# Kernel tuning notes

Measured on AMD Instinct MI355X. Metric: run time of the kernel, lower is better.

Reference implementation:

```python
import jax, jax.numpy as jnp
import numpy as np

B, N, A = 8, 8192, 10   # batch, points, attributes (xyz + normal + 4 extra)
G, M = 512, 32          # num_group, group_size
EPS = 1e-5


def setup_inputs() -> dict:
    key = jax.random.key(0)
    ks = jax.random.split(key, 16)
    w = lambda k, s: jax.random.normal(k, s, jnp.float32) * 0.02
    inp = {"xyz": jax.random.normal(ks[0], (B, N, A), jnp.float32)}
    # Light_T_Net params (conv1 6->64, conv2 64->512, fc 512->36)
    inp["tn_w1"], inp["tn_b1"] = w(ks[1], (64, 6)), jnp.zeros(64, jnp.float32)
    inp["tn_g1"], inp["tn_be1"] = jnp.ones(64, jnp.float32), jnp.zeros(64, jnp.float32)
    inp["tn_w2"], inp["tn_b2"] = w(ks[2], (512, 64)), jnp.zeros(512, jnp.float32)
    inp["tn_g2"], inp["tn_be2"] = jnp.ones(512, jnp.float32), jnp.zeros(512, jnp.float32)
    inp["tn_fw"], inp["tn_fb"] = w(ks[3], (36, 512)), jnp.zeros(36, jnp.float32)
    # Light_PointNet_Encoder convs: A->128->256->512->1024
    for i, (co, ci) in enumerate([(128, A), (256, 128), (512, 256), (1024, 512)], 1):
        inp[f"w{i}"], inp[f"b{i}"] = w(ks[3 + i], (co, ci)), jnp.zeros(co, jnp.float32)
        inp[f"g{i}"], inp[f"be{i}"] = jnp.ones(co, jnp.float32), jnp.zeros(co, jnp.float32)
    return inp


def _bn(x, g, b):
    # training-mode BatchNorm1d: stats over (batch, length) for [BG, n, C]
    m = x.mean((0, 1))
    v = x.var((0, 1))
    return (x - m) * jax.lax.rsqrt(v + EPS) * g + b


def _fps(xyz, npoint):
    # sequential farthest-point sampling (deterministic start index 0)
    coords = xyz[:, :, :3]
    b, n, _ = xyz.shape

    def step(carry, _):
        dist, far = carry
        cen = jnp.take_along_axis(xyz, far[:, None, None], axis=1)  # [B,1,A]
        d = jnp.sum((coords - cen[:, :, :3]) ** 2, -1)              # [B,N]
        dist = jnp.minimum(dist, d)
        return (dist, jnp.argmax(dist, -1)), (far, cen[:, 0, :])

    dist0 = jnp.full((b, n), 1e10, xyz.dtype)
    far0 = jnp.zeros((b,), jnp.int32)
    _, (idx, attrs) = jax.lax.scan(step, (dist0, far0), None, length=npoint)
    return idx.T, attrs.transpose(1, 0, 2)  # [B,G], [B,G,A]


def _forward(xyz, tn_w1, tn_b1, tn_g1, tn_be1, tn_w2, tn_b2, tn_g2, tn_be2,
             tn_fw, tn_fb, w1, b1, g1, be1, w2, b2, g2, be2,
             w3, b3, g3, be3, w4, b4, g4, be4):
    b = xyz.shape[0]
    # ---- Group_for_all_attribute ----
    _, cen = _fps(xyz, G)                                           # [B,G,A]
    # cdist over full attribute dim; squared distance gives identical topk order
    d2 = (jnp.sum(cen ** 2, -1)[:, :, None] + jnp.sum(xyz ** 2, -1)[:, None, :]
          - 2.0 * jnp.einsum('bga,bna->bgn', cen, xyz))             # [B,G,N]
    idx = jax.lax.top_k(-d2, M)[1]                                  # [B,G,M] smallest dists
    nb = xyz[jnp.arange(b)[:, None, None], idx]                     # [B,G,M,A]
    nb = jnp.concatenate([nb[..., :3] - cen[:, :, None, :3], nb[..., 3:]], -1)
    # ---- Light_PointNet_Encoder ----
    pg = nb.reshape(b * G, M, A)
    x6 = pg[:, :, :6]
    # Light_T_Net
    h = jax.nn.relu(_bn(x6 @ tn_w1.T + tn_b1, tn_g1, tn_be1))
    h = jax.nn.relu(_bn(h @ tn_w2.T + tn_b2, tn_g2, tn_be2))
    t = (h.max(1) @ tn_fw.T + tn_fb + jnp.eye(6, dtype=xyz.dtype).reshape(36)).reshape(-1, 6, 6)
    pg = jnp.concatenate([jnp.einsum('bnc,bcd->bnd', x6, t), pg[:, :, 6:]], -1)
    # 1x1 conv stack (= per-point linear) with training-mode BN
    h = jax.nn.relu(_bn(pg @ w1.T + b1, g1, be1))
    h = jax.nn.relu(_bn(h @ w2.T + b2, g2, be2))
    h = jax.nn.relu(_bn(h @ w3.T + b3, g3, be3))
    h = _bn(h @ w4.T + b4, g4, be4)
    return h.max(1).reshape(b, G, -1)                               # [B,G,1024]


def reference(xyz, tn_w1, tn_b1, tn_g1, tn_be1, tn_w2, tn_b2, tn_g2, tn_be2,
              tn_fw, tn_fb, w1, b1, g1, be1, w2, b2, g2, be2,
              w3, b3, g3, be3, w4, b4, g4, be4):
    return _forward(xyz, tn_w1, tn_b1, tn_g1, tn_be1, tn_w2, tn_b2, tn_g2, tn_be2,
                    tn_fw, tn_fb, w1, b1, g1, be1, w2, b2, g2, be2,
                    w3, b3, g3, be3, w4, b4, g4, be4)
```

## Files before the change

kernel.cpp:

```cpp
#include <hip/hip_runtime.h>
#include <hip/hip_bf16.h>

static constexpr int B_  = 8;
static constexpr int N_  = 8192;
static constexpr int A_  = 10;
static constexpr int G_  = 512;
static constexpr int M_  = 32;
static constexpr int S_TOT = B_ * G_ * M_;
static constexpr float EPS_ = 1e-5f;
static constexpr float FMAXV = 3.402823466e+38f;

__device__ __forceinline__ float b2f(__hip_bfloat16 h) { return __bfloat162float(h); }
__device__ __forceinline__ unsigned short f2bs(float f) {
    __hip_bfloat16 h = __float2bfloat16(f);
    return *reinterpret_cast<unsigned short*>(&h);
}

typedef __bf16 bf16x8 __attribute__((ext_vector_type(8)));
typedef float  f32x4  __attribute__((ext_vector_type(4)));

__device__ __forceinline__ unsigned long long shfl_down_u64(unsigned long long v, int off) {
    unsigned lo = (unsigned)v, hi = (unsigned)(v >> 32);
    lo = __shfl_down(lo, off);
    hi = __shfl_down(hi, off);
    return ((unsigned long long)hi << 32) | lo;
}

static constexpr size_t CO_XYZ  = 0;
static constexpr size_t CO_TNW1 = 655360, CO_TNB1 = 655744, CO_TNG1 = 655808, CO_TNBE1 = 655872;
static constexpr size_t CO_TNW2 = 655936, CO_TNB2 = 688704, CO_TNG2 = 689216, CO_TNBE2 = 689728;
static constexpr size_t CO_TNFW = 690240, CO_TNFB = 708672;
static constexpr size_t CO_W1 = 708708, CO_B1 = 709988, CO_G1 = 710116, CO_BE1 = 710244;
static constexpr size_t CO_W2 = 710372, CO_B2 = 743140, CO_G2 = 743396, CO_BE2 = 743652;
static constexpr size_t CO_W3 = 743908, CO_B3 = 874980, CO_G3 = 875492, CO_BE3 = 876004;
static constexpr size_t CO_W4 = 876516, CO_B4 = 1400804, CO_G4 = 1401828, CO_BE4 = 1402852;
static constexpr size_t CO_TOT = 1403876;

static constexpr size_t WB_TNW2 = 0;
static constexpr size_t WB_W2   = 32768;
static constexpr size_t WB_W3   = 65536;
static constexpr size_t WB_W4   = 196608;
static constexpr size_t WB_TOT  = 720896;

#define MB_ (1024ull * 1024ull)
static constexpr size_t OFF_CANON = 0;
static constexpr size_t OFF_CEN   = 6 * MB_;
static constexpr size_t OFF_XSQ   = 6 * MB_ + 256 * 1024;
static constexpr size_t OFF_STATS = 6 * MB_ + 512 * 1024;
static constexpr size_t OFF_COEFF = 6 * MB_ + 576 * 1024;
static constexpr size_t OFF_DUMMY = 6 * MB_ + 640 * 1024;
static constexpr size_t OFF_TMAT  = 6 * MB_ + 768 * 1024;
static constexpr size_t OFF_WBF16 = 8 * MB_;
static constexpr size_t OFF_PG    = 10 * MB_;
static constexpr size_t OFF_TZ1   = 16 * MB_;
static constexpr size_t OFF_TPMAX = 32 * MB_;
static constexpr size_t OFF_TPMIN = 40 * MB_;
static constexpr size_t OFF_Z1    = 16 * MB_;
static constexpr size_t OFF_MM4X  = 16 * MB_;
static constexpr size_t OFF_MM4N  = 32 * MB_;
static constexpr size_t OFF_Z2    = 48 * MB_;
static constexpr size_t OFF_Z3    = 112 * MB_;
static constexpr size_t NEED_A = 240 * MB_;
static constexpr int NCHUNK_ = 8;
static constexpr int CSAMP_  = S_TOT / NCHUNK_;

static constexpr int STF_T1 = 0;
static constexpr int STF_T2 = 128;
static constexpr int STF_M1 = 1152;
static constexpr int STF_M2 = 1408;
static constexpr int STF_M3 = 1920;
static constexpr int STF_M4 = 2944;

struct Ptrs { const void* p[27]; };

__global__ __launch_bounds__(256)
void zero_kernel(float* __restrict__ p, int n)
{
    for (int i = threadIdx.x; i < n; i += 256) p[i] = 0.f;
}

__global__ __launch_bounds__(256)
void convert_kernel(Ptrs ptrs, float* __restrict__ canon)
{
    const size_t gid = (size_t)blockIdx.x * 256 + threadIdx.x;
    if (gid >= CO_TOT) return;
    constexpr size_t offs[28] = {0, 655360, 655744, 655808, 655872, 655936,
        688704, 689216, 689728, 690240, 708672, 708708, 709988, 710116, 710244,
        710372, 743140, 743396, 743652, 743908, 874980, 875492, 876004, 876516,
        1400804, 1401828, 1402852, 1403876};
    int j = 0;
    while (j < 26 && gid >= offs[j + 1]) ++j;
    const size_t loc = gid - offs[j];
    const bool fp32m = (((const unsigned short*)ptrs.p[3])[0] == 0);
    float v;
    if (fp32m) v = ((const float*)ptrs.p[j])[loc];
    else       v = b2f(((const __hip_bfloat16*)ptrs.p[j])[loc]);
    canon[gid] = v;
}

__global__ __launch_bounds__(256)
void wconv_kernel(const float* __restrict__ canon, __hip_bfloat16* __restrict__ wb)
{
    const size_t gid = (size_t)blockIdx.x * 256 + threadIdx.x;
    if (gid >= WB_TOT) return;
    constexpr size_t offs[5] = {0, 32768, 65536, 196608, 720896};
    constexpr size_t co[4]   = {CO_TNW2, CO_W2, CO_W3, CO_W4};
    int j = 0;
    while (j < 3 && gid >= offs[j + 1]) ++j;
    wb[gid] = __float2bfloat16(canon[co[j] + (gid - offs[j])]);
}

__global__ __launch_bounds__(512)
void fps_kernel(const float* __restrict__ xyz, float* __restrict__ cen)
{
    __shared__ unsigned long long red[2][8];
    __shared__ int fidx[G_];

    const int t = threadIdx.x;
    const int b = blockIdx.x;
    const float* xb = xyz + (size_t)b * N_ * A_;

    float px[16], py[16], pz[16], dist[16];
#pragma unroll
    for (int j = 0; j < 16; ++j) {
        const int i = j * 512 + t;
        px[j] = xb[(size_t)i * A_ + 0];
        py[j] = xb[(size_t)i * A_ + 1];
        pz[j] = xb[(size_t)i * A_ + 2];
        dist[j] = 1e10f;
    }
    __syncthreads();

    int far = 0;
    for (int it = 0; it < G_; ++it) {
        if (t == 0) fidx[it] = far;
        const float2 cxy = *reinterpret_cast<const float2*>(xb + (size_t)far * A_);
        const float  cz  = xb[(size_t)far * A_ + 2];

        unsigned long long best = 0;
#pragma unroll
        for (int j = 0; j < 16; ++j) {
            const float dx = px[j] - cxy.x, dy = py[j] - cxy.y, dz = pz[j] - cz;
            const float d = dx * dx + dy * dy + dz * dz;
            const float nd = fminf(dist[j], d);
            dist[j] = nd;
            const unsigned long long pk =
                ((unsigned long long)__float_as_uint(nd) << 32) |
                (unsigned)~(unsigned)(j * 512 + t);
            best = (pk > best) ? pk : best;
        }
#pragma unroll
        for (int off = 32; off; off >>= 1) {
            const unsigned long long o = shfl_down_u64(best, off);
            best = (o > best) ? o : best;
        }
        if ((t & 63) == 0) red[it & 1][t >> 6] = best;
        __syncthreads();
        unsigned long long m = red[it & 1][0];
#pragma unroll
        for (int w = 1; w < 8; ++w) {
            const unsigned long long o = red[it & 1][w];
            m = (o > m) ? o : m;
        }
        far = (int)(~(unsigned)m);
    }
    __syncthreads();
    for (int e = t; e < G_ * A_; e += 512) {
        const int it = e / A_;
        const int a  = e - it * A_;
        cen[((size_t)b * G_ + it) * A_ + a] = xb[(size_t)fidx[it] * A_ + a];
    }
}

__global__ __launch_bounds__(256)
void xsq_kernel(const float* __restrict__ xyz, float* __restrict__ xsq)
{
    const int i = blockIdx.x * 256 + threadIdx.x;
    float s = 0.f;
#pragma unroll
    for (int a = 0; a < A_; ++a) { const float v = xyz[(size_t)i * A_ + a]; s += v * v; }
    xsq[i] = s;
}

__global__ __launch_bounds__(256)
void knn_kernel(const float* __restrict__ xyz, const float* __restrict__ cen,
                const float* __restrict__ xsq, float* __restrict__ pg)
{
    __shared__ float d2[N_];
    __shared__ float ca[A_];
    __shared__ float csqs;
    __shared__ float redV[4];
    __shared__ int   redI[4];
    __shared__ int   win[M_];
    __shared__ int   curwin;

    const int t  = threadIdx.x;
    const int bg = blockIdx.x;
    const int b  = bg >> 9;
    const float* xb  = xyz + (size_t)b * N_ * A_;
    const float* xsb = xsq + (size_t)b * N_;

    if (t < A_) ca[t] = cen[(size_t)bg * A_ + t];
    __syncthreads();
    if (t == 0) {
        float s = 0.f;
        for (int a = 0; a < A_; ++a) s += ca[a] * ca[a];
        csqs = s;
    }
    __syncthreads();
    const float csq = csqs;

    for (int j = 0; j < 32; ++j) {
        const int i = j * 256 + t;
        float dot = 0.f;
#pragma unroll
        for (int a = 0; a < A_; ++a) dot += xb[(size_t)i * A_ + a] * ca[a];
        d2[i] = (csq + xsb[i]) - 2.f * dot;
    }
    __syncthreads();

    float bv = FMAXV; int bi = 0;
    for (int j = 0; j < 32; ++j) {
        const int i = j * 256 + t;
        const float v = d2[i];
        if (v < bv) { bv = v; bi = i; }
    }

    for (int it = 0; it < M_; ++it) {
        float rv = bv; int ri = bi;
#pragma unroll
        for (int off = 32; off; off >>= 1) {
            const float ov = __shfl_down(rv, off);
            const int   oi = __shfl_down(ri, off);
            if (ov < rv || (ov == rv && oi < ri)) { rv = ov; ri = oi; }
        }
        if ((t & 63) == 0) { redV[t >> 6] = rv; redI[t >> 6] = ri; }
        __syncthreads();
        if (t == 0) {
            float v = redV[0]; int wi = redI[0];
            for (int w = 1; w < 4; ++w)
                if (redV[w] < v || (redV[w] == v && redI[w] < wi)) { v = redV[w]; wi = redI[w]; }
            win[it] = wi; curwin = wi; d2[wi] = FMAXV;
        }
        __syncthreads();
        const int wi = curwin;
        if ((wi & 255) == t) {
            bv = FMAXV; bi = 0;
            for (int j = 0; j < 32; ++j) {
                const int i = j * 256 + t;
                const float v = d2[i];
                if (v < bv) { bv = v; bi = i; }
            }
        }
    }
    __syncthreads();
    if (t < M_) {
        const int i = win[t];
        for (int a = 0; a < A_; ++a) {
            float v = xb[(size_t)i * A_ + a];
            if (a < 3) v -= ca[a];
            pg[((size_t)bg * M_ + t) * A_ + a] = v;
        }
    }
}

template<int K, int C>
__global__ __launch_bounds__(256)
void mlp_small_kernel(const float* __restrict__ pgx,
                      const float* __restrict__ W,
                      const float* __restrict__ Bv,
                      __hip_bfloat16* __restrict__ Zout,
                      float* __restrict__ stats)
{
    __shared__ float w[C * K];
    __shared__ float bb[C];
    __shared__ float lstat[C][2];
    const int t = threadIdx.x;
    for (int i = t; i < C * K; i += 256) w[i] = W[i];
    for (int i = t; i < C; i += 256) bb[i] = Bv[i];
    for (int i = t; i < 2 * C; i += 256) ((float*)lstat)[i] = 0.f;
    __syncthreads();

    const size_t s = (size_t)blockIdx.x * 256 + t;
    float x[K];
#pragma unroll
    for (int k = 0; k < K; ++k) x[k] = pgx[s * A_ + k];

    ushort4 u;
    for (int c = 0; c < C; ++c) {
        float z = bb[c];
#pragma unroll
        for (int k = 0; k < K; ++k) z += w[c * K + k] * x[k];
        const unsigned short zs = f2bs(z);
        const int cm = c & 3;
        if (cm == 0) u.x = zs; else if (cm == 1) u.y = zs; else if (cm == 2) u.z = zs;
        else { u.w = zs; *reinterpret_cast<ushort4*>(Zout + s * C + (c - 3)) = u; }

        float sv = z, sq = z * z;
#pragma unroll
        for (int off = 32; off; off >>= 1) {
            sv += __shfl_down(sv, off);
            sq += __shfl_down(sq, off);
        }
        if ((t & 63) == 0) { atomicAdd(&lstat[c][0], sv); atomicAdd(&lstat[c][1], sq); }
    }
    __syncthreads();
    for (int c = t; c < C; c += 256) {
        atomicAdd(&stats[c],     lstat[c][0]);
        atomicAdd(&stats[C + c], lstat[c][1]);
    }
}

__global__ __launch_bounds__(256)
void finalize_kernel(const float* __restrict__ stats, const float* __restrict__ g,
                     const float* __restrict__ be, float* __restrict__ coeff, int C)
{
    for (int c = threadIdx.x; c < C; c += 256) {
        const float mean = stats[c] * (1.f / (float)S_TOT);
        const float var  = stats[C + c] * (1.f / (float)S_TOT) - mean * mean;
        const float sc = g[c] * rsqrtf(fmaxf(var, 0.f) + EPS_);
        coeff[c]     = sc;
        coeff[C + c] = be[c] - mean * sc;
    }
}

template<int K, int N, bool POOL>
__global__ __launch_bounds__(256)
void gemm_mfma_kernel(const __hip_bfloat16* __restrict__ Zin,
                      const float* __restrict__ coeff,
                      const __hip_bfloat16* __restrict__ Wb,
                      const float* __restrict__ Bv,
                      __hip_bfloat16* __restrict__ Zout,
                      float* __restrict__ maxbuf,
                      float* __restrict__ minbuf,
                      float* __restrict__ stats)
{
    constexpr int PITCH = 72;
    __shared__ __hip_bfloat16 As[128 * PITCH];
    __shared__ __hip_bfloat16 Bs[128 * PITCH];
    __shared__ float csc[K];
    __shared__ float csh[K];
    __shared__ float lstat[256];

    const int t    = threadIdx.x;
    const int lane = t & 63;
    const int wave = t >> 6;
    const int wm   = wave >> 1;
    const int wn   = wave & 1;
    const int ln   = lane & 15;
    const int quad = lane >> 4;
    const int c0   = blockIdx.x * 128;
    const int s0   = blockIdx.y * 128;

    for (int i = t; i < K; i += 256) { csc[i] = coeff[i]; csh[i] = coeff[K + i]; }
    lstat[t] = 0.f;

    f32x4 acc[4][4];
#pragma unroll
    for (int ni = 0; ni < 4; ++ni) {
        const float bj = Bv[c0 + wn * 64 + ni * 16 + ln];
#pragma unroll
        for (int mi = 0; mi < 4; ++mi) acc[mi][ni] = (f32x4){bj, bj, bj, bj};
    }

    for (int kt = 0; kt < K; kt += 64) {
        __syncthreads();
#pragma unroll
        for (int p = 0; p < 4; ++p) {
            const int id = p * 256 + t;
            const int r  = id >> 3;
            const int sg = id & 7;
            const float4 raw = *reinterpret_cast<const float4*>(
                Zin + (size_t)(s0 + r) * K + kt + sg * 8);
            const __hip_bfloat162* p2 = reinterpret_cast<const __hip_bfloat162*>(&raw);
            unsigned short tmp[8] __attribute__((aligned(16)));
#pragma unroll
            for (int j = 0; j < 4; ++j) {
                const int k0 = kt + sg * 8 + 2 * j;
                const float x0 = fmaxf(b2f(p2[j].x) * csc[k0]     + csh[k0],     0.f);
                const float x1 = fmaxf(b2f(p2[j].y) * csc[k0 + 1] + csh[k0 + 1], 0.f);
                tmp[2 * j]     = f2bs(x0);
                tmp[2 * j + 1] = f2bs(x1);
            }
            *reinterpret_cast<float4*>(&As[r * PITCH + sg * 8]) =
                *reinterpret_cast<const float4*>(tmp);
            *reinterpret_cast<float4*>(&Bs[r * PITCH + sg * 8]) =
                *reinterpret_cast<const float4*>(Wb + (size_t)(c0 + r) * K + kt + sg * 8);
        }
        __syncthreads();

        bf16x8 af[4][2], bf_[4][2];
#pragma unroll
        for (int mi = 0; mi < 4; ++mi)
#pragma unroll
            for (int kk = 0; kk < 2; ++kk)
                af[mi][kk] = *reinterpret_cast<const bf16x8*>(
                    &As[(wm * 64 + mi * 16 + ln) * PITCH + quad * 8 + kk * 32]);
#pragma unroll
        for (int ni = 0; ni < 4; ++ni)
#pragma unroll
            for (int kk = 0; kk < 2; ++kk)
                bf_[ni][kk] = *reinterpret_cast<const bf16x8*>(
                    &Bs[(wn * 64 + ni * 16 + ln) * PITCH + quad * 8 + kk * 32]);
#pragma unroll
        for (int kk = 0; kk < 2; ++kk)
#pragma unroll
            for (int mi = 0; mi < 4; ++mi)
#pragma unroll
                for (int ni = 0; ni < 4; ++ni)
                    acc[mi][ni] = __builtin_amdgcn_mfma_f32_16x16x32_bf16(
                        af[mi][kk], bf_[ni][kk], acc[mi][ni], 0, 0, 0);
    }

#pragma unroll
    for (int ni = 0; ni < 4; ++ni) {
        float sv = 0.f, sq = 0.f;
#pragma unroll
        for (int mi = 0; mi < 4; ++mi)
#pragma unroll
            for (int r = 0; r < 4; ++r) {
                const float v = acc[mi][ni][r];
                sv += v; sq += v * v;
            }
        sv += __shfl_xor(sv, 16); sq += __shfl_xor(sq, 16);
        sv += __shfl_xor(sv, 32); sq += __shfl_xor(sq, 32);
        if (quad == 0) {
            const int col = wn * 64 + ni * 16 + ln;
            atomicAdd(&lstat[col], sv);
            atomicAdd(&lstat[128 + col], sq);
        }
    }
    __syncthreads();
    if (t < 128) {
        atomicAdd(&stats[c0 + t],     lstat[t]);
        atomicAdd(&stats[N + c0 + t], lstat[128 + t]);
    }

    if constexpr (POOL) {
#pragma unroll
        for (int ni = 0; ni < 4; ++ni) {
            float mx0 = -FMAXV, mn0 = FMAXV, mx1 = -FMAXV, mn1 = FMAXV;
#pragma unroll
            for (int mi = 0; mi < 2; ++mi)
#pragma unroll
                for (int r = 0; r < 4; ++r) {
                    const float v = acc[mi][ni][r];
                    mx0 = fmaxf(mx0, v); mn0 = fminf(mn0, v);
                }
#pragma unroll
            for (int mi = 2; mi < 4; ++mi)
#pragma unroll
                for (int r = 0; r < 4; ++r) {
                    const float v = acc[mi][ni][r];
                    mx1 = fmaxf(mx1, v); mn1 = fminf(mn1, v);
                }
            mx0 = fmaxf(mx0, __shfl_xor(mx0, 16)); mn0 = fminf(mn0, __shfl_xor(mn0, 16));
            mx0 = fmaxf(mx0, __shfl_xor(mx0, 32)); mn0 = fminf(mn0, __shfl_xor(mn0, 32));
            mx1 = fmaxf(mx1, __shfl_xor(mx1, 16)); mn1 = fminf(mn1, __shfl_xor(mn1, 16));
            mx1 = fmaxf(mx1, __shfl_xor(mx1, 32)); mn1 = fminf(mn1, __shfl_xor(mn1, 32));
            if (quad == 0) {
                const int col = c0 + wn * 64 + ni * 16 + ln;
                const int g   = (s0 >> 5) + wm * 2;
                maxbuf[(size_t)g * N + col]       = mx0;
                minbuf[(size_t)g * N + col]       = mn0;
                maxbuf[(size_t)(g + 1) * N + col] = mx1;
                minbuf[(size_t)(g + 1) * N + col] = mn1;
            }
        }
    } else {
#pragma unroll
        for (int mi = 0; mi < 4; ++mi)
#pragma unroll
            for (int r = 0; r < 4; ++r) {
                const size_t row = (size_t)(s0 + wm * 64 + mi * 16 + quad * 4 + r);
#pragma unroll
                for (int ni = 0; ni < 4; ++ni) {
                    const int col = c0 + wn * 64 + ni * 16 + ln;
                    Zout[row * N + col] = __float2bfloat16(acc[mi][ni][r]);
                }
            }
    }
}

__global__ __launch_bounds__(64)
void tnet_fc_kernel(const float* __restrict__ maxbuf, const float* __restrict__ minbuf,
                    const float* __restrict__ coeff, const float* __restrict__ FW,
                    const float* __restrict__ FB, float* __restrict__ tmat)
{
    __shared__ float h[512];
    const int bg = blockIdx.x;
    const int t  = threadIdx.x;
    for (int i = t; i < 512; i += 64) {
        const float sc = coeff[i], sh = coeff[512 + i];
        const float v = (sc >= 0.f) ? maxbuf[(size_t)bg * 512 + i] : minbuf[(size_t)bg * 512 + i];
        h[i] = fmaxf(sc * v + sh, 0.f);
    }
    __syncthreads();
    if (t < 36) {
        float acc = FB[t] + ((t % 7 == 0) ? 1.f : 0.f);
        for (int k = 0; k < 512; ++k) acc += FW[t * 512 + k] * h[k];
        tmat[(size_t)bg * 36 + t] = acc;
    }
}

__global__ __launch_bounds__(256)
void transform_kernel(float* __restrict__ pg, const float* __restrict__ tmat)
{
    const size_t s = (size_t)blockIdx.x * 256 + threadIdx.x;
    const int bg = (int)(s >> 5);
    float x[6];
#pragma unroll
    for (int c = 0; c < 6; ++c) x[c] = pg[s * A_ + c];
    const float* tm = tmat + (size_t)bg * 36;
#pragma unroll
    for (int d = 0; d < 6; ++d) {
        float o = 0.f;
#pragma unroll
        for (int c = 0; c < 6; ++c) o += x[c] * tm[c * 6 + d];
        pg[s * A_ + d] = o;
    }
}

__global__ __launch_bounds__(256)
void output_kernel(const float* __restrict__ maxbuf, const float* __restrict__ minbuf,
                   const float* __restrict__ coeff, const unsigned short* __restrict__ probe,
                   void* __restrict__ out)
{
    const size_t e = (size_t)blockIdx.x * 256 + threadIdx.x;
    const int c = (int)(e & 1023);
    const float sc = coeff[c], sh = coeff[1024 + c];
    const float v = (sc >= 0.f) ? maxbuf[e] : minbuf[e];
    const float r = sc * v + sh;
    if (probe[0] == 0) ((float*)out)[e] = r;
    else ((__hip_bfloat16*)out)[e] = __float2bfloat16(r);
}

extern "C" void kernel_launch(void* const* d_in, const int* in_sizes, int n_in,
                              void* d_out, int out_size, void* d_ws, size_t ws_size,
                              hipStream_t stream)
{
    char* ws = (char*)d_ws;
    float*          canon = (float*)(ws + OFF_CANON);
    float*          cen   = (float*)(ws + OFF_CEN);
    float*          xsq   = (float*)(ws + OFF_XSQ);
    float*          stats = (float*)(ws + OFF_STATS);
    float*          coeff = (float*)(ws + OFF_COEFF);
    float*          dummy = (float*)(ws + OFF_DUMMY);
    float*          tmat  = (float*)(ws + OFF_TMAT);
    __hip_bfloat16* wbf   = (__hip_bfloat16*)(ws + OFF_WBF16);
    float*          tpmax = (float*)(ws + OFF_TPMAX);
    float*          tpmin = (float*)(ws + OFF_TPMIN);
    float*          pg    = (float*)(ws + OFF_PG);
    __hip_bfloat16* tz1   = (__hip_bfloat16*)(ws + OFF_TZ1);
    __hip_bfloat16* z1    = (__hip_bfloat16*)(ws + OFF_Z1);
    __hip_bfloat16* z2    = (__hip_bfloat16*)(ws + OFF_Z2);
    __hip_bfloat16* z3    = (__hip_bfloat16*)(ws + OFF_Z3);
    float*          mmax4 = (float*)(ws + OFF_MM4X);
    float*          mmin4 = (float*)(ws + OFF_MM4N);

    Ptrs ptrs;
    for (int i = 0; i < 27; ++i) ptrs.p[i] = d_in[i];

    const float* cxyz = canon + CO_XYZ;

    zero_kernel<<<1, 256, 0, stream>>>(stats, 5120);
    convert_kernel<<<(int)((CO_TOT + 255) / 256), 256, 0, stream>>>(ptrs, canon);
    wconv_kernel<<<(int)((WB_TOT + 255) / 256), 256, 0, stream>>>(canon, wbf);

    fps_kernel<<<B_, 512, 0, stream>>>(cxyz, cen);
    xsq_kernel<<<(B_ * N_) / 256, 256, 0, stream>>>(cxyz, xsq);
    knn_kernel<<<B_ * G_, 256, 0, stream>>>(cxyz, cen, xsq, pg);

    mlp_small_kernel<6, 64><<<S_TOT / 256, 256, 0, stream>>>(
        pg, canon + CO_TNW1, canon + CO_TNB1, tz1, stats + STF_T1);
    finalize_kernel<<<1, 256, 0, stream>>>(stats + STF_T1, canon + CO_TNG1, canon + CO_TNBE1,
                                           coeff + STF_T1, 64);
    gemm_mfma_kernel<64, 512, true><<<dim3(4, S_TOT / 128), 256, 0, stream>>>(
        tz1, coeff + STF_T1, wbf + WB_TNW2, canon + CO_TNB2, nullptr, tpmax, tpmin, stats + STF_T2);
    finalize_kernel<<<1, 256, 0, stream>>>(stats + STF_T2, canon + CO_TNG2, canon + CO_TNBE2,
                                           coeff + STF_T2, 512);
    tnet_fc_kernel<<<B_ * G_, 64, 0, stream>>>(tpmax, tpmin, coeff + STF_T2,
                                               canon + CO_TNFW, canon + CO_TNFB, tmat);
    transform_kernel<<<S_TOT / 256, 256, 0, stream>>>(pg, tmat);

    mlp_small_kernel<10, 128><<<S_TOT / 256, 256, 0, stream>>>(
        pg, canon + CO_W1, canon + CO_B1, z1, stats + STF_M1);
    finalize_kernel<<<1, 256, 0, stream>>>(stats + STF_M1, canon + CO_G1, canon + CO_BE1,
                                           coeff + STF_M1, 128);
    gemm_mfma_kernel<128, 256, false><<<dim3(2, S_TOT / 128), 256, 0, stream>>>(
        z1, coeff + STF_M1, wbf + WB_W2, canon + CO_B2, z2, nullptr, nullptr, stats + STF_M2);
    finalize_kernel<<<1, 256, 0, stream>>>(stats + STF_M2, canon + CO_G2, canon + CO_BE2,
                                           coeff + STF_M2, 256);

    if (ws_size >= NEED_A) {
        gemm_mfma_kernel<256, 512, false><<<dim3(4, S_TOT / 128), 256, 0, stream>>>(
            z2, coeff + STF_M2, wbf + WB_W3, canon + CO_B3, z3, nullptr, nullptr, stats + STF_M3);
        finalize_kernel<<<1, 256, 0, stream>>>(stats + STF_M3, canon + CO_G3, canon + CO_BE3,
                                               coeff + STF_M3, 512);
        gemm_mfma_kernel<512, 1024, true><<<dim3(8, S_TOT / 128), 256, 0, stream>>>(
            z3, coeff + STF_M3, wbf + WB_W4, canon + CO_B4, nullptr, mmax4, mmin4, stats + STF_M4);
    } else {
        for (int c = 0; c < NCHUNK_; ++c) {
            gemm_mfma_kernel<256, 512, false><<<dim3(4, CSAMP_ / 128), 256, 0, stream>>>(
                z2 + (size_t)c * CSAMP_ * 256, coeff + STF_M2, wbf + WB_W3, canon + CO_B3,
                z3, nullptr, nullptr, stats + STF_M3);
        }
        finalize_kernel<<<1, 256, 0, stream>>>(stats + STF_M3, canon + CO_G3, canon + CO_BE3,
                                               coeff + STF_M3, 512);
        for (int c = 0; c < NCHUNK_; ++c) {
            gemm_mfma_kernel<256, 512, false><<<dim3(4, CSAMP_ / 128), 256, 0, stream>>>(
                z2 + (size_t)c * CSAMP_ * 256, coeff + STF_M2, wbf + WB_W3, canon + CO_B3,
                z3, nullptr, nullptr, dummy);
            gemm_mfma_kernel<512, 1024, true><<<dim3(8, CSAMP_ / 128), 256, 0, stream>>>(
                z3, coeff + STF_M3, wbf + WB_W4, canon + CO_B4, nullptr,
                mmax4 + (size_t)(c * CSAMP_ / 32) * 1024,
                mmin4 + (size_t)(c * CSAMP_ / 32) * 1024, stats + STF_M4);
        }
    }
    finalize_kernel<<<1, 256, 0, stream>>>(stats + STF_M4, canon + CO_G4, canon + CO_BE4,
                                           coeff + STF_M4, 1024);

    output_kernel<<<(B_ * G_ * 1024) / 256, 256, 0, stream>>>(
        mmax4, mmin4, coeff + STF_M4, (const unsigned short*)d_in[3], d_out);
}
```

Measured before the change: 1.600 ms.

## Batch two FPS clouds per block and split BN stats out of small MLP

The FPS kernel now handles two batches per block, interleaving their distance updates, and carries the winning point's coordinates through the shuffle and shared-memory reductions. This removes the dependent global load of the centroid on each iteration and gives the sequential loop more independent work to hide latency. The small MLP kernels no longer do per-channel wave reductions and atomics for BatchNorm statistics. A separate stats kernel now reads back the bf16 outputs, so the statistics come from rounded values and cost an extra pass over memory. FPS also runs on half as many blocks, using more registers per thread.

```diff
diff --git a/kernel.cpp b/kernel.cpp
--- a/kernel.cpp
+++ b/kernel.cpp
@@ -113,62 +113,109 @@
 __global__ __launch_bounds__(512)
 void fps_kernel(const float* __restrict__ xyz, float* __restrict__ cen)
 {
-    __shared__ unsigned long long red[2][8];
-    __shared__ int fidx[G_];
+    __shared__ unsigned long long rK[2][2][8];
+    __shared__ float rX[2][2][8], rY[2][2][8], rZ[2][2][8];
+    __shared__ int fidx[2][G_];
 
     const int t = threadIdx.x;
-    const int b = blockIdx.x;
-    const float* xb = xyz + (size_t)b * N_ * A_;
-
-    float px[16], py[16], pz[16], dist[16];
+    const float* xb0 = xyz + (size_t)(2 * blockIdx.x)     * N_ * A_;
+    const float* xb1 = xyz + (size_t)(2 * blockIdx.x + 1) * N_ * A_;
+
+    float px0[16], py0[16], pz0[16], d0[16];
+    float px1[16], py1[16], pz1[16], d1[16];
 #pragma unroll
     for (int j = 0; j < 16; ++j) {
         const int i = j * 512 + t;
-        px[j] = xb[(size_t)i * A_ + 0];
-        py[j] = xb[(size_t)i * A_ + 1];
-        pz[j] = xb[(size_t)i * A_ + 2];
-        dist[j] = 1e10f;
-    }
-    __syncthreads();
-
-    int far = 0;
+        px0[j] = xb0[(size_t)i * A_ + 0];
+        py0[j] = xb0[(size_t)i * A_ + 1];
+        pz0[j] = xb0[(size_t)i * A_ + 2];
+        px1[j] = xb1[(size_t)i * A_ + 0];
+        py1[j] = xb1[(size_t)i * A_ + 1];
+        pz1[j] = xb1[(size_t)i * A_ + 2];
+        d0[j] = 1e10f; d1[j] = 1e10f;
+    }
+
+    int far0 = 0, far1 = 0;
+    float cx0 = xb0[0], cy0 = xb0[1], cz0 = xb0[2];
+    float cx1 = xb1[0], cy1 = xb1[1], cz1 = xb1[2];
+
     for (int it = 0; it < G_; ++it) {
-        if (t == 0) fidx[it] = far;
-        const float2 cxy = *reinterpret_cast<const float2*>(xb + (size_t)far * A_);
-        const float  cz  = xb[(size_t)far * A_ + 2];
-
-        unsigned long long best = 0;
+        if (t == 0) fidx[0][it] = far0;
+        if (t == 1) fidx[1][it] = far1;
+
+        unsigned long long b0 = 0, b1 = 0;
 #pragma unroll
         for (int j = 0; j < 16; ++j) {
-            const float dx = px[j] - cxy.x, dy = py[j] - cxy.y, dz = pz[j] - cz;
-            const float d = dx * dx + dy * dy + dz * dz;
-            const float nd = fminf(dist[j], d);
-            dist[j] = nd;
+            const float ax = px0[j] - cx0, ay = py0[j] - cy0, az = pz0[j] - cz0;
+            const float nd = fminf(d0[j], ax * ax + ay * ay + az * az);
+            d0[j] = nd;
             const unsigned long long pk =
                 ((unsigned long long)__float_as_uint(nd) << 32) |
                 (unsigned)~(unsigned)(j * 512 + t);
-            best = (pk > best) ? pk : best;
+            b0 = (pk > b0) ? pk : b0;
+        }
+#pragma unroll
+        for (int j = 0; j < 16; ++j) {
+            const float ax = px1[j] - cx1, ay = py1[j] - cy1, az = pz1[j] - cz1;
+            const float nd = fminf(d1[j], ax * ax + ay * ay + az * az);
+            d1[j] = nd;
+            const unsigned long long pk =
+                ((unsigned long long)__float_as_uint(nd) << 32) |
+                (unsigned)~(unsigned)(j * 512 + t);
+            b1 = (pk > b1) ? pk : b1;
+        }
+        const int bj0 = (int)((~(unsigned)b0) >> 9) & 15;
+        const int bj1 = (int)((~(unsigned)b1) >> 9) & 15;
+        float bx0 = px0[0], by0 = py0[0], bz0 = pz0[0];
+        float bx1 = px1[0], by1 = py1[0], bz1 = pz1[0];
+#pragma unroll
+        for (int j = 1; j < 16; ++j) {
+            if (bj0 == j) { bx0 = px0[j]; by0 = py0[j]; bz0 = pz0[j]; }
+            if (bj1 == j) { bx1 = px1[j]; by1 = py1[j]; bz1 = pz1[j]; }
         }
 #pragma unroll
         for (int off = 32; off; off >>= 1) {
-            const unsigned long long o = shfl_down_u64(best, off);
-            best = (o > best) ? o : best;
-        }
-        if ((t & 63) == 0) red[it & 1][t >> 6] = best;
+            const unsigned long long o0 = shfl_down_u64(b0, off);
+            const float ox0 = __shfl_down(bx0, off), oy0 = __shfl_down(by0, off),
+                        oz0 = __shfl_down(bz0, off);
+            if (o0 > b0) { b0 = o0; bx0 = ox0; by0 = oy0; bz0 = oz0; }
+            const unsigned long long o1 = shfl_down_u64(b1, off);
+            const float ox1 = __shfl_down(bx1, off), oy1 = __shfl_down(by1, off),
+                        oz1 = __shfl_down(bz1, off);
+            if (o1 > b1) { b1 = o1; bx1 = ox1; by1 = oy1; bz1 = oz1; }
+        }
+        const int p = it & 1;
+        if ((t & 63) == 0) {
+            const int w = t >> 6;
+            rK[p][0][w] = b0; rX[p][0][w] = bx0; rY[p][0][w] = by0; rZ[p][0][w] = bz0;
+            rK[p][1][w] = b1; rX[p][1][w] = bx1; rY[p][1][w] = by1; rZ[p][1][w] = bz1;
+        }
         __syncthreads();
-        unsigned long long m = red[it & 1][0];
+        unsigned long long m0 = rK[p][0][0];
+        float mx0 = rX[p][0][0], my0 = rY[p][0][0], mz0 = rZ[p][0][0];
+        unsigned long long m1 = rK[p][1][0];
+        float mx1 = rX[p][1][0], my1 = rY[p][1][0], mz1 = rZ[p][1][0];
 #pragma unroll
         for (int w = 1; w < 8; ++w) {
-            const unsigned long long o = red[it & 1][w];
-            m = (o > m) ? o : m;
-        }
-        far = (int)(~(unsigned)m);
-    }
-    __syncthreads();
-    for (int e = t; e < G_ * A_; e += 512) {
-        const int it = e / A_;
-        const int a  = e - it * A_;
-        cen[((size_t)b * G_ + it) * A_ + a] = xb[(size_t)fidx[it] * A_ + a];
+            const unsigned long long o0 = rK[p][0][w];
+            if (o0 > m0) { m0 = o0; mx0 = rX[p][0][w]; my0 = rY[p][0][w]; mz0 = rZ[p][0][w]; }
+            const unsigned long long o1 = rK[p][1][w];
+            if (o1 > m1) { m1 = o1; mx1 = rX[p][1][w]; my1 = rY[p][1][w]; mz1 = rZ[p][1][w]; }
+        }
+        far0 = (int)(~(unsigned)m0) & (N_ - 1);
+        far1 = (int)(~(unsigned)m1) & (N_ - 1);
+        cx0 = mx0; cy0 = my0; cz0 = mz0;
+        cx1 = mx1; cy1 = my1; cz1 = mz1;
+    }
+    __syncthreads();
+    for (int e = t; e < 2 * G_ * A_; e += 512) {
+        const int bb = e / (G_ * A_);
+        const int r  = e - bb * (G_ * A_);
+        const int it = r / A_;
+        const int a  = r - it * A_;
+        const float* x = bb ? xb1 : xb0;
+        cen[((size_t)(2 * blockIdx.x + bb) * G_ + it) * A_ + a] =
+            x[(size_t)fidx[bb][it] * A_ + a];
     }
 }
 
@@ -269,16 +316,13 @@
 void mlp_small_kernel(const float* __restrict__ pgx,
                       const float* __restrict__ W,
                       const float* __restrict__ Bv,
-                      __hip_bfloat16* __restrict__ Zout,
-                      float* __restrict__ stats)
+                      __hip_bfloat16* __restrict__ Zout)
 {
     __shared__ float w[C * K];
     __shared__ float bb[C];
-    __shared__ float lstat[C][2];
     const int t = threadIdx.x;
     for (int i = t; i < C * K; i += 256) w[i] = W[i];
     for (int i = t; i < C; i += 256) bb[i] = Bv[i];
-    for (int i = t; i < 2 * C; i += 256) ((float*)lstat)[i] = 0.f;
     __syncthreads();
 
     const size_t s = (size_t)blockIdx.x * 256 + t;
@@ -287,6 +331,7 @@
     for (int k = 0; k < K; ++k) x[k] = pgx[s * A_ + k];
 
     ushort4 u;
+#pragma unroll 4
     for (int c = 0; c < C; ++c) {
         float z = bb[c];
 #pragma unroll
@@ -295,19 +340,33 @@
         const int cm = c & 3;
         if (cm == 0) u.x = zs; else if (cm == 1) u.y = zs; else if (cm == 2) u.z = zs;
         else { u.w = zs; *reinterpret_cast<ushort4*>(Zout + s * C + (c - 3)) = u; }
-
-        float sv = z, sq = z * z;
-#pragma unroll
-        for (int off = 32; off; off >>= 1) {
-            sv += __shfl_down(sv, off);
-            sq += __shfl_down(sq, off);
-        }
-        if ((t & 63) == 0) { atomicAdd(&lstat[c][0], sv); atomicAdd(&lstat[c][1], sq); }
-    }
-    __syncthreads();
-    for (int c = t; c < C; c += 256) {
-        atomicAdd(&stats[c],     lstat[c][0]);
-        atomicAdd(&stats[C + c], lstat[c][1]);
+    }
+}
+
+template<int C>
+__global__ __launch_bounds__(256)
+void stats_kernel(const __hip_bfloat16* __restrict__ Z, float* __restrict__ stats)
+{
+    __shared__ float ls[2 * C];
+    constexpr int L = 256 / C;
+    const int t   = threadIdx.x;
+    const int c   = t & (C - 1);
+    const int sub = t / C;
+    for (int i = t; i < 2 * C; i += 256) ls[i] = 0.f;
+    __syncthreads();
+
+    float sv = 0.f, sq = 0.f;
+    const size_t s0 = (size_t)blockIdx.x * 1024;
+    for (int k = 0; k < 1024 / L; ++k) {
+        const float v = b2f(Z[(s0 + sub + (size_t)k * L) * C + c]);
+        sv += v; sq += v * v;
+    }
+    atomicAdd(&ls[c], sv);
+    atomicAdd(&ls[C + c], sq);
+    __syncthreads();
+    for (int i = t; i < C; i += 256) {
+        atomicAdd(&stats[i],     ls[i]);
+        atomicAdd(&stats[C + i], ls[C + i]);
     }
 }
 
@@ -567,12 +626,13 @@
     convert_kernel<<<(int)((CO_TOT + 255) / 256), 256, 0, stream>>>(ptrs, canon);
     wconv_kernel<<<(int)((WB_TOT + 255) / 256), 256, 0, stream>>>(canon, wbf);
 
-    fps_kernel<<<B_, 512, 0, stream>>>(cxyz, cen);
+    fps_kernel<<<B_ / 2, 512, 0, stream>>>(cxyz, cen);
     xsq_kernel<<<(B_ * N_) / 256, 256, 0, stream>>>(cxyz, xsq);
     knn_kernel<<<B_ * G_, 256, 0, stream>>>(cxyz, cen, xsq, pg);
 
     mlp_small_kernel<6, 64><<<S_TOT / 256, 256, 0, stream>>>(
-        pg, canon + CO_TNW1, canon + CO_TNB1, tz1, stats + STF_T1);
+        pg, canon + CO_TNW1, canon + CO_TNB1, tz1);
+    stats_kernel<64><<<S_TOT / 1024, 256, 0, stream>>>(tz1, stats + STF_T1);
     finalize_kernel<<<1, 256, 0, stream>>>(stats + STF_T1, canon + CO_TNG1, canon + CO_TNBE1,
                                            coeff + STF_T1, 64);
     gemm_mfma_kernel<64, 512, true><<<dim3(4, S_TOT / 128), 256, 0, stream>>>(
@@ -584,7 +644,8 @@
     transform_kernel<<<S_TOT / 256, 256, 0, stream>>>(pg, tmat);
 
     mlp_small_kernel<10, 128><<<S_TOT / 256, 256, 0, stream>>>(
-        pg, canon + CO_W1, canon + CO_B1, z1, stats + STF_M1);
+        pg, canon + CO_W1, canon + CO_B1, z1);
+    stats_kernel<128><<<S_TOT / 1024, 256, 0, stream>>>(z1, stats + STF_M1);
     finalize_kernel<<<1, 256, 0, stream>>>(stats + STF_M1, canon + CO_G1, canon + CO_BE1,
                                            coeff + STF_M1, 128);
     gemm_mfma_kernel<128, 256, false><<<dim3(2, S_TOT / 128), 256, 0, stream>>>(
```

Measured after the change: 2.888 ms. 80.5% more time.
